# Optimization experiments

Hardware: AMD Instinct MI355X
Metric: run time of the kernel (lower is better)

The kernel has to match this reference:

```python
import jax, jax.numpy as jnp
import numpy as np

D_MODEL = 4096
NUM_HEADS = 64
DEPTH = D_MODEL // NUM_HEADS  # 64
B = 64   # must equal NUM_HEADS (quirk of original rope-after-split-heads code)
S = 64   # must equal NUM_HEADS (S*DEPTH must equal D_MODEL)


def setup_inputs() -> dict:
    key = jax.random.key(0)
    ks = jax.random.split(key, 9)
    scale = 1.0 / np.sqrt(D_MODEL)
    d = {"x": jax.random.normal(ks[0], (B, S, D_MODEL), dtype=jnp.float32)}
    for i, n in enumerate(["q", "k", "v", "o"]):
        d[f"w_{n}"] = jax.random.normal(ks[1 + i], (D_MODEL, D_MODEL), dtype=jnp.float32) * scale
        d[f"b_{n}"] = jax.random.normal(ks[5 + i], (D_MODEL,), dtype=jnp.float32) * 0.01
    return d


def _rope(x):
    # Faithful to the original: rope is applied to (B, H, S, depth) and treats
    # dim 1 (heads) as the 'sequence' axis, with inv_freq sized for full d_model.
    inv_freq = 1.0 / (10000.0 ** (jnp.arange(0, D_MODEL, 2, dtype=jnp.float32) / D_MODEL))
    pos = jnp.arange(x.shape[1], dtype=jnp.float32)[:, None]       # (H, 1)
    sinusoid = pos * inv_freq                                       # (H, d_model/2)
    sin = jnp.sin(sinusoid)[None, :, None, :]                       # (1, H, 1, d_model/2)
    cos = jnp.cos(sinusoid)[None, :, None, :]
    xr = x.reshape(x.shape[0], x.shape[1], -1, 2)                   # (B, H, S*depth/2, 2)
    real, imag = xr[..., 0], xr[..., 1]                             # (B, H, M) with M == d_model/2
    rot_real = real * cos - imag * sin                              # broadcasts to (1, B, H, M)
    rot_imag = real * sin + imag * cos
    return jnp.stack((rot_real, rot_imag), axis=-1).reshape(x.shape)


def reference(x, w_q, b_q, w_k, b_k, w_v, b_v, w_o, b_o):
    def split_heads(t):  # (B, S, d_model) -> (B, H, S, depth)
        return t.reshape(B, S, NUM_HEADS, DEPTH).transpose(0, 2, 1, 3)

    q = split_heads(x @ w_q.T + b_q)
    k = split_heads(x @ w_k.T + b_k)
    v = split_heads(x @ w_v.T + b_v)
    q = _rope(q)
    k = _rope(k)

    scores = jnp.einsum("bhqd,bhkd->bhqk", q, k) / np.sqrt(DEPTH).astype(np.float32)
    weights = jax.nn.softmax(scores, axis=-1)
    out = jnp.einsum("bhqk,bhkd->bhqd", weights, v)
    out = out.transpose(0, 2, 1, 3).reshape(B, S, D_MODEL)
    return out @ w_o.T + b_o
```

## Files before the change

### kernel.cpp

```cpp
#include <hip/hip_runtime.h>
#include <cstdint>
#include <cstddef>


typedef _Float16 half8 __attribute__((ext_vector_type(8)));
typedef float floatx4 __attribute__((ext_vector_type(4)));

#define NELT_W 16777216u
#define NEG_LOG2_10000_OVER_2048 (-0.0064881408103278559f)

__device__ __forceinline__ void gl_lds16(const void* g, void* l) {
    __builtin_amdgcn_global_load_lds(
        (const __attribute__((address_space(1))) void*)(void*)g,
        (__attribute__((address_space(3))) void*)l,
        16, 0, 0);
}

__global__ __launch_bounds__(256) void cast5_kernel(
    const float* __restrict__ x,  const float* __restrict__ wq,
    const float* __restrict__ wk, const float* __restrict__ wv,
    const float* __restrict__ wo,
    _Float16* __restrict__ xh, _Float16* __restrict__ wcat,
    _Float16* __restrict__ woh)
{
    const float* s;
    _Float16* d;
    switch (blockIdx.y) {
        case 0:  s = x;  d = xh;                 break;
        case 1:  s = wq; d = wcat;               break;
        case 2:  s = wk; d = wcat + NELT_W;      break;
        case 3:  s = wv; d = wcat + 2 * NELT_W;  break;
        default: s = wo; d = woh;                break;
    }
    int i0 = (blockIdx.x * 256 + threadIdx.x) * 8;
    int stride = gridDim.x * 256 * 8;
    for (int i = i0; i < (int)NELT_W; i += stride) {
        const float4 a = *(const float4*)(s + i);
        const float4 b = *(const float4*)(s + i + 4);
        half8 h;
        h[0] = (_Float16)a.x; h[1] = (_Float16)a.y;
        h[2] = (_Float16)a.z; h[3] = (_Float16)a.w;
        h[4] = (_Float16)b.x; h[5] = (_Float16)b.y;
        h[6] = (_Float16)b.z; h[7] = (_Float16)b.w;
        *(half8*)(d + i) = h;
    }
}

__global__ __launch_bounds__(256) void biascat_kernel(
    const float* __restrict__ bq, const float* __restrict__ bk,
    const float* __restrict__ bv, float* __restrict__ out)
{
    int i = blockIdx.x * 256 + threadIdx.x;
    if (i < 4096) {
        out[i]        = bq[i];
        out[4096 + i] = bk[i];
        out[8192 + i] = bv[i];
    }
}

template <int OUT_F16>
__global__ __launch_bounds__(256, 2) void gemm_nt_kernel(
    const _Float16* __restrict__ A, const _Float16* __restrict__ B,
    const float* __restrict__ bias, void* __restrict__ Cout,
    int M, int N, int K)
{
    __shared__ __align__(16) _Float16 As[128 * 32];
    __shared__ __align__(16) _Float16 Bs[128 * 32];

    const int tid  = threadIdx.x;
    const int col0 = blockIdx.x * 128;
    const int row0 = blockIdx.y * 128;
    const int wave = tid >> 6;
    const int lane = tid & 63;
    const int wm = (wave >> 1) * 64;
    const int wn = (wave & 1) * 64;

    floatx4 zero = {0.f, 0.f, 0.f, 0.f};
    floatx4 acc[4][4];
#pragma unroll
    for (int i = 0; i < 4; i++)
#pragma unroll
        for (int j = 0; j < 4; j++) acc[i][j] = zero;

    const int ar = tid >> 2;
    const int ac = (((tid & 3) - (ar >> 1)) & 3) * 8;
    const _Float16* Ag0 = A + (size_t)(row0 + ar) * K + ac;
    const _Float16* Ag1 = A + (size_t)(row0 + 64 + ar) * K + ac;
    const _Float16* Bg0 = B + (size_t)(col0 + ar) * K + ac;
    const _Float16* Bg1 = B + (size_t)(col0 + 64 + ar) * K + ac;
    _Float16* As0 = As + tid * 8;
    _Float16* As1 = As + (tid + 256) * 8;
    _Float16* Bs0 = Bs + tid * 8;
    _Float16* Bs1 = Bs + (tid + 256) * 8;

    const int fr = lane & 15;
    const int kc = lane >> 4;

    for (int kt = 0; kt < K; kt += 32) {
        gl_lds16(Ag0 + kt, As0);
        gl_lds16(Ag1 + kt, As1);
        gl_lds16(Bg0 + kt, Bs0);
        gl_lds16(Bg1 + kt, Bs1);
        __syncthreads();

        half8 af[4], bf[4];
#pragma unroll
        for (int t = 0; t < 4; t++) {
            const int rowa = wm + t * 16 + fr;
            const int rowb = wn + t * 16 + fr;
            const int pa = ((kc + (rowa >> 1)) & 3) * 8;
            const int pb = ((kc + (rowb >> 1)) & 3) * 8;
            af[t] = *(const half8*)(As + (size_t)rowa * 32 + pa);
            bf[t] = *(const half8*)(Bs + (size_t)rowb * 32 + pb);
        }
#pragma unroll
        for (int i = 0; i < 4; i++)
#pragma unroll
            for (int j = 0; j < 4; j++)
                acc[i][j] = __builtin_amdgcn_mfma_f32_16x16x32_f16(
                    af[i], bf[j], acc[i][j], 0, 0, 0);
        __syncthreads();
    }

    const int crow = row0 + wm + ((lane >> 4) << 2);
    const int ccol = col0 + wn + (lane & 15);
#pragma unroll
    for (int i = 0; i < 4; i++) {
#pragma unroll
        for (int j = 0; j < 4; j++) {
            const int gc = ccol + j * 16;
            const float bv = bias[gc];
#pragma unroll
            for (int r2 = 0; r2 < 4; r2++) {
                const int gr = crow + i * 16 + r2;
                const float v = acc[i][j][r2] + bv;
                if (OUT_F16)
                    ((_Float16*)Cout)[(size_t)gr * N + gc] = (_Float16)v;
                else
                    ((float*)Cout)[(size_t)gr * N + gc] = v;
            }
        }
    }
}

__global__ __launch_bounds__(256) void attn_kernel(
    const _Float16* __restrict__ qkv, _Float16* __restrict__ out)
{
    __shared__ __align__(16) _Float16 qs[64][72];
    __shared__ __align__(16) _Float16 ks[64][72];
    __shared__ __align__(16) _Float16 vt[64][72];
    __shared__ __align__(16) _Float16 ps[4][16][72];

    const int tid  = threadIdx.x;
    const int bb   = blockIdx.x >> 6;
    const int hh   = blockIdx.x & 63;
    const int wave = tid >> 6;
    const int lane = tid & 63;
    const int r  = tid >> 2;
    const int cb = (tid & 3) * 8;
    const float fb = (float)bb;

    const _Float16* grow = qkv + (size_t)(bb * 64 + r) * 12288 + hh * 64;

#pragma unroll
    for (int u = 0; u < 2; u++) {
        const int c8 = cb + u * 32;
        half8 q8 = *(const half8*)(grow + c8);
        half8 k8 = *(const half8*)(grow + 4096 + c8);
        half8 v8 = *(const half8*)(grow + 8192 + c8);
#pragma unroll
        for (int p = 0; p < 4; p++) {
            const int m = r * 32 + (c8 >> 1) + p;
            const float theta = fb * exp2f((float)m * NEG_LOG2_10000_OVER_2048);
            float sn, cs;
            __sincosf(theta, &sn, &cs);
            const float qe = (float)q8[2 * p], qo = (float)q8[2 * p + 1];
            q8[2 * p]     = (_Float16)(qe * cs - qo * sn);
            q8[2 * p + 1] = (_Float16)(qe * sn + qo * cs);
            const float ke = (float)k8[2 * p], ko = (float)k8[2 * p + 1];
            k8[2 * p]     = (_Float16)(ke * cs - ko * sn);
            k8[2 * p + 1] = (_Float16)(ke * sn + ko * cs);
        }
        *(half8*)&qs[r][c8] = q8;
        *(half8*)&ks[r][c8] = k8;
#pragma unroll
        for (int j = 0; j < 8; j++) vt[c8 + j][r] = v8[j];
    }
    __syncthreads();

    const int fr = lane & 15;
    const int fc = (lane >> 4) * 8;

    floatx4 sa[4];
#pragma unroll
    for (int t = 0; t < 4; t++) sa[t] = (floatx4){0.f, 0.f, 0.f, 0.f};
    half8 a0 = *(const half8*)&qs[wave * 16 + fr][fc];
    half8 a1 = *(const half8*)&qs[wave * 16 + fr][fc + 32];
#pragma unroll
    for (int t = 0; t < 4; t++) {
        half8 kb0 = *(const half8*)&ks[t * 16 + fr][fc];
        half8 kb1 = *(const half8*)&ks[t * 16 + fr][fc + 32];
        sa[t] = __builtin_amdgcn_mfma_f32_16x16x32_f16(a0, kb0, sa[t], 0, 0, 0);
        sa[t] = __builtin_amdgcn_mfma_f32_16x16x32_f16(a1, kb1, sa[t], 0, 0, 0);
    }

#pragma unroll
    for (int i = 0; i < 4; i++) {
        float mx = -1e30f;
#pragma unroll
        for (int t = 0; t < 4; t++) mx = fmaxf(mx, sa[t][i]);
#pragma unroll
        for (int d = 1; d < 16; d <<= 1) mx = fmaxf(mx, __shfl_xor(mx, d));
        float sum = 0.f;
        float pv[4];
#pragma unroll
        for (int t = 0; t < 4; t++) {
            const float e = __expf((sa[t][i] - mx) * 0.125f);
            pv[t] = e;
            sum += e;
        }
#pragma unroll
        for (int d = 1; d < 16; d <<= 1) sum += __shfl_xor(sum, d);
        const float inv = 1.0f / sum;
        const int prow = ((lane >> 4) << 2) + i;
#pragma unroll
        for (int t = 0; t < 4; t++)
            ps[wave][prow][t * 16 + fr] = (_Float16)(pv[t] * inv);
    }

    half8 pa0 = *(const half8*)&ps[wave][fr][fc];
    half8 pa1 = *(const half8*)&ps[wave][fr][fc + 32];
    floatx4 oa[4];
#pragma unroll
    for (int t = 0; t < 4; t++) oa[t] = (floatx4){0.f, 0.f, 0.f, 0.f};
#pragma unroll
    for (int t = 0; t < 4; t++) {
        half8 vb0 = *(const half8*)&vt[t * 16 + fr][fc];
        half8 vb1 = *(const half8*)&vt[t * 16 + fr][fc + 32];
        oa[t] = __builtin_amdgcn_mfma_f32_16x16x32_f16(pa0, vb0, oa[t], 0, 0, 0);
        oa[t] = __builtin_amdgcn_mfma_f32_16x16x32_f16(pa1, vb1, oa[t], 0, 0, 0);
    }

    _Float16* obase = out + (size_t)(bb * 64) * 4096 + hh * 64;
#pragma unroll
    for (int t = 0; t < 4; t++)
#pragma unroll
        for (int i = 0; i < 4; i++) {
            const int sq = wave * 16 + ((lane >> 4) << 2) + i;
            obase[(size_t)sq * 4096 + t * 16 + fr] = (_Float16)oa[t][i];
        }
}

extern "C" void kernel_launch(void* const* d_in, const int* in_sizes, int n_in,
                              void* d_out, int out_size, void* d_ws, size_t ws_size,
                              hipStream_t stream)
{
    const float* x  = (const float*)d_in[0];
    const float* wq = (const float*)d_in[1];
    const float* bq = (const float*)d_in[2];
    const float* wk = (const float*)d_in[3];
    const float* bk = (const float*)d_in[4];
    const float* wv = (const float*)d_in[5];
    const float* bv = (const float*)d_in[6];
    const float* wo = (const float*)d_in[7];
    const float* bo = (const float*)d_in[8];

    const size_t NELT = (size_t)4096 * 4096;
    char* ws = (char*)d_ws;
    _Float16* xh      = (_Float16*)(ws);
    _Float16* wcat    = (_Float16*)(ws + 33554432);
    _Float16* woh     = (_Float16*)(ws + 134217728);
    _Float16* qkv     = (_Float16*)(ws + 167772160);
    _Float16* attnbuf = (_Float16*)(ws + 268435456);
    float*    biascat = (float*)(ws + 301989888);

    cast5_kernel<<<dim3(1024, 5), dim3(256), 0, stream>>>(
        x, wq, wk, wv, wo, xh, wcat, woh);
    biascat_kernel<<<dim3(16), dim3(256), 0, stream>>>(bq, bk, bv, biascat);

    gemm_nt_kernel<1><<<dim3(96, 32), dim3(256), 0, stream>>>(
        xh, wcat, biascat, qkv, 4096, 12288, 4096);

    attn_kernel<<<dim3(4096), dim3(256), 0, stream>>>(qkv, attnbuf);

    gemm_nt_kernel<0><<<dim3(32, 32), dim3(256), 0, stream>>>(
        attnbuf, woh, bo, d_out, 4096, 4096, 4096);
}
```

Before: 1.003 ms.

## Use 32x32 MFMA in GEMM, XCD-aware block mapping, and row-major V in attention

The GEMM kernel switches from 16x16x32 to 32x32x16 MFMA tiles, cutting the LDS fragment loads per k-step and issuing fewer, larger matrix instructions. It also replaces the 2D grid with a 1D grid remapped so each XCD owns a contiguous band of output columns, aiming for better L2 reuse of the B operand. Separately, the attention kernel stores V row-major instead of transposing it at load time, and gathers the transposed fragments with scalar LDS reads at MFMA time, which may add bank-conflicted reads.

```diff
diff --git a/kernel.cpp b/kernel.cpp
--- a/kernel.cpp
+++ b/kernel.cpp
@@ -5,6 +5,7 @@
 
 typedef _Float16 half8 __attribute__((ext_vector_type(8)));
 typedef float floatx4 __attribute__((ext_vector_type(4)));
+typedef float floatx16 __attribute__((ext_vector_type(16)));
 
 #define NELT_W 16777216u
 #define NEG_LOG2_10000_OVER_2048 (-0.0064881408103278559f)
@@ -67,20 +68,26 @@
     __shared__ __align__(16) _Float16 As[128 * 32];
     __shared__ __align__(16) _Float16 Bs[128 * 32];
 
-    const int tid  = threadIdx.x;
-    const int col0 = blockIdx.x * 128;
-    const int row0 = blockIdx.y * 128;
+    const int tid = threadIdx.x;
+    const int flat = blockIdx.x;
+    const int xcd  = flat & 7;
+    const int k5   = flat >> 3;
+    const int colPerXcd = N >> 10;
+    const int col0 = (xcd * colPerXcd + (k5 >> 5)) << 7;
+    const int row0 = (k5 & 31) << 7;
+
     const int wave = tid >> 6;
     const int lane = tid & 63;
     const int wm = (wave >> 1) * 64;
     const int wn = (wave & 1) * 64;
 
-    floatx4 zero = {0.f, 0.f, 0.f, 0.f};
-    floatx4 acc[4][4];
-#pragma unroll
-    for (int i = 0; i < 4; i++)
-#pragma unroll
-        for (int j = 0; j < 4; j++) acc[i][j] = zero;
+    floatx16 acc[2][2];
+#pragma unroll
+    for (int i = 0; i < 2; i++)
+#pragma unroll
+        for (int j = 0; j < 2; j++)
+#pragma unroll
+            for (int r = 0; r < 16; r++) acc[i][j][r] = 0.f;
 
     const int ar = tid >> 2;
     const int ac = (((tid & 3) - (ar >> 1)) & 3) * 8;
@@ -93,8 +100,8 @@
     _Float16* Bs0 = Bs + tid * 8;
     _Float16* Bs1 = Bs + (tid + 256) * 8;
 
-    const int fr = lane & 15;
-    const int kc = lane >> 4;
+    const int m31   = lane & 31;
+    const int khalf = lane >> 5;
 
     for (int kt = 0; kt < K; kt += 32) {
         gl_lds16(Ag0 + kt, As0);
@@ -103,37 +110,42 @@
         gl_lds16(Bg1 + kt, Bs1);
         __syncthreads();
 
-        half8 af[4], bf[4];
-#pragma unroll
-        for (int t = 0; t < 4; t++) {
-            const int rowa = wm + t * 16 + fr;
-            const int rowb = wn + t * 16 + fr;
-            const int pa = ((kc + (rowa >> 1)) & 3) * 8;
-            const int pb = ((kc + (rowb >> 1)) & 3) * 8;
-            af[t] = *(const half8*)(As + (size_t)rowa * 32 + pa);
-            bf[t] = *(const half8*)(Bs + (size_t)rowb * 32 + pb);
-        }
-#pragma unroll
-        for (int i = 0; i < 4; i++)
-#pragma unroll
-            for (int j = 0; j < 4; j++)
-                acc[i][j] = __builtin_amdgcn_mfma_f32_16x16x32_f16(
-                    af[i], bf[j], acc[i][j], 0, 0, 0);
+        half8 af[2][2], bf[2][2];
+#pragma unroll
+        for (int s = 0; s < 2; s++) {
+            const int c = s * 2 + khalf;
+#pragma unroll
+            for (int t = 0; t < 2; t++) {
+                const int rowa = wm + t * 32 + m31;
+                const int rowb = wn + t * 32 + m31;
+                const int pa = ((c + (rowa >> 1)) & 3) * 8;
+                const int pb = ((c + (rowb >> 1)) & 3) * 8;
+                af[t][s] = *(const half8*)(As + (size_t)rowa * 32 + pa);
+                bf[t][s] = *(const half8*)(Bs + (size_t)rowb * 32 + pb);
+            }
+        }
+#pragma unroll
+        for (int s = 0; s < 2; s++)
+#pragma unroll
+            for (int i = 0; i < 2; i++)
+#pragma unroll
+                for (int j = 0; j < 2; j++)
+                    acc[i][j] = __builtin_amdgcn_mfma_f32_32x32x16_f16(
+                        af[i][s], bf[j][s], acc[i][j], 0, 0, 0);
         __syncthreads();
     }
 
-    const int crow = row0 + wm + ((lane >> 4) << 2);
-    const int ccol = col0 + wn + (lane & 15);
-#pragma unroll
-    for (int i = 0; i < 4; i++) {
-#pragma unroll
-        for (int j = 0; j < 4; j++) {
-            const int gc = ccol + j * 16;
+    const int rbase = (lane >> 5) * 4;
+#pragma unroll
+    for (int i = 0; i < 2; i++) {
+#pragma unroll
+        for (int j = 0; j < 2; j++) {
+            const int gc = col0 + wn + j * 32 + m31;
             const float bv = bias[gc];
 #pragma unroll
-            for (int r2 = 0; r2 < 4; r2++) {
-                const int gr = crow + i * 16 + r2;
-                const float v = acc[i][j][r2] + bv;
+            for (int r = 0; r < 16; r++) {
+                const int gr = row0 + wm + i * 32 + (r & 3) + 8 * (r >> 2) + rbase;
+                const float v = acc[i][j][r] + bv;
                 if (OUT_F16)
                     ((_Float16*)Cout)[(size_t)gr * N + gc] = (_Float16)v;
                 else
@@ -148,7 +160,7 @@
 {
     __shared__ __align__(16) _Float16 qs[64][72];
     __shared__ __align__(16) _Float16 ks[64][72];
-    __shared__ __align__(16) _Float16 vt[64][72];
+    __shared__ __align__(16) _Float16 vs[64][72];
     __shared__ __align__(16) _Float16 ps[4][16][72];
 
     const int tid  = threadIdx.x;
@@ -183,8 +195,7 @@
         }
         *(half8*)&qs[r][c8] = q8;
         *(half8*)&ks[r][c8] = k8;
-#pragma unroll
-        for (int j = 0; j < 8; j++) vt[c8 + j][r] = v8[j];
+        *(half8*)&vs[r][c8] = v8;
     }
     __syncthreads();
 
@@ -228,17 +239,22 @@
             ps[wave][prow][t * 16 + fr] = (_Float16)(pv[t] * inv);
     }
 
-    half8 pa0 = *(const half8*)&ps[wave][fr][fc];
-    half8 pa1 = *(const half8*)&ps[wave][fr][fc + 32];
+    half8 pa[2];
+    pa[0] = *(const half8*)&ps[wave][fr][fc];
+    pa[1] = *(const half8*)&ps[wave][fr][fc + 32];
     floatx4 oa[4];
 #pragma unroll
     for (int t = 0; t < 4; t++) oa[t] = (floatx4){0.f, 0.f, 0.f, 0.f};
 #pragma unroll
     for (int t = 0; t < 4; t++) {
-        half8 vb0 = *(const half8*)&vt[t * 16 + fr][fc];
-        half8 vb1 = *(const half8*)&vt[t * 16 + fr][fc + 32];
-        oa[t] = __builtin_amdgcn_mfma_f32_16x16x32_f16(pa0, vb0, oa[t], 0, 0, 0);
-        oa[t] = __builtin_amdgcn_mfma_f32_16x16x32_f16(pa1, vb1, oa[t], 0, 0, 0);
+#pragma unroll
+        for (int u = 0; u < 2; u++) {
+            const int kb = u * 32 + fc;
+            half8 vb;
+#pragma unroll
+            for (int j = 0; j < 8; j++) vb[j] = vs[kb + j][t * 16 + fr];
+            oa[t] = __builtin_amdgcn_mfma_f32_16x16x32_f16(pa[u], vb, oa[t], 0, 0, 0);
+        }
     }
 
     _Float16* obase = out + (size_t)(bb * 64) * 4096 + hh * 64;
@@ -278,11 +294,11 @@
         x, wq, wk, wv, wo, xh, wcat, woh);
     biascat_kernel<<<dim3(16), dim3(256), 0, stream>>>(bq, bk, bv, biascat);
 
-    gemm_nt_kernel<1><<<dim3(96, 32), dim3(256), 0, stream>>>(
+    gemm_nt_kernel<1><<<dim3(3072), dim3(256), 0, stream>>>(
         xh, wcat, biascat, qkv, 4096, 12288, 4096);
 
     attn_kernel<<<dim3(4096), dim3(256), 0, stream>>>(qkv, attnbuf);
 
-    gemm_nt_kernel<0><<<dim3(32, 32), dim3(256), 0, stream>>>(
+    gemm_nt_kernel<0><<<dim3(1024), dim3(256), 0, stream>>>(
         attnbuf, woh, bo, d_out, 4096, 4096, 4096);
 }
```

After: 1.064 ms. +6.1%, slower.
